# Optimization experiments

Measured on AMD Instinct MI355X. Metric: run time of the kernel, lower is better.

## Reference

```python
import jax, jax.numpy as jnp
import numpy as np

E = 1024
H = 16
D = E // H  # head dim = 64


def _moe(x, Wexp, bexp, Wg, bg):
    # x: (m, s, e); Wexp: (3, e, o); bexp: (3, o); Wg: (e, 3); bg: (3,)
    gate = jax.nn.softmax(jnp.einsum('mse,en->msn', x, Wg) + bg, axis=-1)  # (m,s,3)
    expert_out = jnp.einsum('mse,neo->msno', x, Wexp) + bexp               # (m,s,3,o)
    return jnp.einsum('msn,msno->mso', gate, expert_out)


def setup_inputs() -> dict:
    key = jax.random.key(0)
    ks = jax.random.split(key, 10)
    m, s = 4, 2048
    sc = 1.0 / np.sqrt(E)
    inp = {'x': jax.random.normal(ks[0], (m, s, E), jnp.float32)}
    for i, p in enumerate(['q', 'k', 'v']):
        inp['W' + p] = jax.random.normal(ks[1 + 3 * i], (3, E, E), jnp.float32) * sc
        inp['b' + p] = jnp.zeros((3, E), jnp.float32)
        inp['Wg' + p] = jax.random.normal(ks[2 + 3 * i], (E, 3), jnp.float32) * sc
        inp['bg' + p] = jnp.zeros((3,), jnp.float32)
    return inp


def reference(x, Wq, bq, Wgq, bgq, Wk, bk, Wgk, bgk, Wv, bv, Wgv, bgv):
    m, s, e = x.shape
    xq = _moe(x, Wq, bq, Wgq, bgq).reshape(m, s, H, D).transpose(0, 2, 1, 3)  # (m,H,s,D)
    xk = _moe(x, Wk, bk, Wgk, bgk).reshape(m, s, H, D).transpose(0, 2, 1, 3)
    xv = _moe(x, Wv, bv, Wgv, bgv).reshape(m, s, H, D).transpose(0, 2, 1, 3)
    scores = jnp.einsum('mhqd,mhkd->mhqk', xq, xk) / jnp.float32(np.sqrt(D))
    attn = jax.nn.softmax(scores, axis=-1)
    out = jnp.einsum('mhqk,mhkd->mhqd', attn, xv)
    return out.transpose(0, 2, 1, 3).reshape(m, s, e)
```

## Files before the change

kernel.cpp:

```cpp
#include <hip/hip_runtime.h>
#include <math.h>

#define T_TOK 8192
#define E_DIM 1024
#define S_LEN 2048

typedef _Float16 f16x4 __attribute__((ext_vector_type(4)));
typedef _Float16 f16x8 __attribute__((ext_vector_type(8)));
typedef float f32x16 __attribute__((ext_vector_type(16)));

__device__ __forceinline__ void async16(const void* g, void* l) {
  __builtin_amdgcn_global_load_lds(
      (const __attribute__((address_space(1))) void*)g,
      (__attribute__((address_space(3))) void*)l, 16, 0, 0);
}

__global__ __launch_bounds__(64) void gates_kernel(
    const float* __restrict__ x,
    const float* __restrict__ Wgq, const float* __restrict__ bgq,
    const float* __restrict__ Wgk, const float* __restrict__ bgk,
    const float* __restrict__ Wgv, const float* __restrict__ bgv,
    float* __restrict__ gates) {
  const int t = blockIdx.x;
  const int lane = threadIdx.x;
  const float* xr = x + (size_t)t * E_DIM;
  float acc[9];
#pragma unroll
  for (int i = 0; i < 9; ++i) acc[i] = 0.f;
  for (int e = lane; e < E_DIM; e += 64) {
    const float xv = xr[e];
    acc[0] = fmaf(xv, Wgq[e * 3 + 0], acc[0]);
    acc[1] = fmaf(xv, Wgq[e * 3 + 1], acc[1]);
    acc[2] = fmaf(xv, Wgq[e * 3 + 2], acc[2]);
    acc[3] = fmaf(xv, Wgk[e * 3 + 0], acc[3]);
    acc[4] = fmaf(xv, Wgk[e * 3 + 1], acc[4]);
    acc[5] = fmaf(xv, Wgk[e * 3 + 2], acc[5]);
    acc[6] = fmaf(xv, Wgv[e * 3 + 0], acc[6]);
    acc[7] = fmaf(xv, Wgv[e * 3 + 1], acc[7]);
    acc[8] = fmaf(xv, Wgv[e * 3 + 2], acc[8]);
  }
#pragma unroll
  for (int off = 32; off > 0; off >>= 1) {
#pragma unroll
    for (int i = 0; i < 9; ++i) acc[i] += __shfl_down(acc[i], off, 64);
  }
  if (lane == 0) {
    const float* bg[3] = {bgq, bgk, bgv};
#pragma unroll
    for (int p = 0; p < 3; ++p) {
      float z0 = acc[p * 3 + 0] + bg[p][0];
      float z1 = acc[p * 3 + 1] + bg[p][1];
      float z2 = acc[p * 3 + 2] + bg[p][2];
      float mx = fmaxf(z0, fmaxf(z1, z2));
      float e0 = expf(z0 - mx), e1 = expf(z1 - mx), e2 = expf(z2 - mx);
      float inv = 1.f / (e0 + e1 + e2);
      float* gp = gates + ((size_t)p * T_TOK + t) * 3;
      gp[0] = e0 * inv;
      gp[1] = e1 * inv;
      gp[2] = e2 * inv;
    }
  }
}

__global__ __launch_bounds__(256) void split_x_kernel(
    const float* __restrict__ x, _Float16* __restrict__ xh, _Float16* __restrict__ xl) {
  const size_t i = ((size_t)blockIdx.x * 256 + threadIdx.x) * 4;
  const float4 v = *(const float4*)(x + i);
  f16x4 h, lo;
  h[0] = (_Float16)v.x; lo[0] = (_Float16)(v.x - (float)h[0]);
  h[1] = (_Float16)v.y; lo[1] = (_Float16)(v.y - (float)h[1]);
  h[2] = (_Float16)v.z; lo[2] = (_Float16)(v.z - (float)h[2]);
  h[3] = (_Float16)v.w; lo[3] = (_Float16)(v.w - (float)h[3]);
  *(f16x4*)(xh + i) = h;
  *(f16x4*)(xl + i) = lo;
}

__global__ __launch_bounds__(256) void split_w_kernel(
    const float* __restrict__ Wq, const float* __restrict__ Wk, const float* __restrict__ Wv,
    _Float16* __restrict__ wh, _Float16* __restrict__ wl) {
  const int mat = blockIdx.y;
  const float* W = ((mat < 3) ? Wq : (mat < 6) ? Wk : Wv) + (size_t)(mat % 3) * 1048576;
  const int kt = (blockIdx.x >> 4) * 64, ct = (blockIdx.x & 15) * 64;
  __shared__ _Float16 hs[64][72];
  __shared__ _Float16 ls[64][72];
  const int tid = threadIdx.x;
#pragma unroll
  for (int i = 0; i < 4; ++i) {
    const int r = (tid >> 4) + i * 16;
    const int c4 = (tid & 15) * 4;
    const float4 v = *(const float4*)(W + (size_t)(kt + r) * 1024 + ct + c4);
    _Float16 h;
    h = (_Float16)v.x; hs[c4 + 0][r] = h; ls[c4 + 0][r] = (_Float16)(v.x - (float)h);
    h = (_Float16)v.y; hs[c4 + 1][r] = h; ls[c4 + 1][r] = (_Float16)(v.y - (float)h);
    h = (_Float16)v.z; hs[c4 + 2][r] = h; ls[c4 + 2][r] = (_Float16)(v.z - (float)h);
    h = (_Float16)v.w; hs[c4 + 3][r] = h; ls[c4 + 3][r] = (_Float16)(v.w - (float)h);
  }
  __syncthreads();
#pragma unroll
  for (int i = 0; i < 2; ++i) {
    const int u = tid + i * 256;
    const int c = u >> 3, seg = u & 7;
    const size_t o = (size_t)mat * 1048576 + (size_t)(ct + c) * 1024 + kt + seg * 8;
    *(f16x8*)(wh + o) = *(const f16x8*)(&hs[c][seg * 8]);
    *(f16x8*)(wl + o) = *(const f16x8*)(&ls[c][seg * 8]);
  }
}

__global__ __launch_bounds__(256, 2) void moe_mfma_kernel(
    const _Float16* __restrict__ xh, const _Float16* __restrict__ xl,
    const _Float16* __restrict__ wh, const _Float16* __restrict__ wl,
    const float* __restrict__ bq_, const float* __restrict__ bk_, const float* __restrict__ bv_,
    const float* __restrict__ gates,
    float* __restrict__ oq_, float* __restrict__ ok_, float* __restrict__ ov_) {
  const int p = blockIdx.z;
  const float* bias = (p == 0) ? bq_ : (p == 1) ? bk_ : bv_;
  float* out = (p == 0) ? oq_ : (p == 1) ? ok_ : ov_;

  __shared__ _Float16 Ah[128][32], Al[128][32], Bh[128][32], Bl[128][32];
  __shared__ float gsh[128][3];
  __shared__ float bsh[3][128];

  const int tid = threadIdx.x;
  const int l = tid & 63, w = tid >> 6;
  const int wm = w & 1, wn = w >> 1;
  const int row0 = blockIdx.x * 128, col0 = blockIdx.y * 128;

  for (int i = tid; i < 384; i += 256)
    gsh[i / 3][i % 3] = gates[((size_t)p * T_TOK + row0 + i / 3) * 3 + (i % 3)];
  for (int i = tid; i < 384; i += 256)
    bsh[i >> 7][i & 127] = bias[(i >> 7) * 1024 + col0 + (i & 127)];

  const int m = l & 31, half = l >> 5;
  const int S = (m >> 1) & 3;
  const int rr = l >> 2;
  const int gc = (l & 3) ^ ((l >> 3) & 3);
  const size_t aoff = (size_t)(row0 + w * 32 + rr) * 1024 + gc * 8;

  f32x16 fin[2][2];
#pragma unroll
  for (int i = 0; i < 2; ++i)
#pragma unroll
    for (int j = 0; j < 2; ++j)
#pragma unroll
      for (int r = 0; r < 16; ++r) fin[i][j][r] = 0.f;

  for (int e = 0; e < 3; ++e) {
    f32x16 acc[2][2];
#pragma unroll
    for (int i = 0; i < 2; ++i)
#pragma unroll
      for (int j = 0; j < 2; ++j)
#pragma unroll
        for (int r = 0; r < 16; ++r) acc[i][j][r] = 0.f;

    const size_t wbase = ((size_t)(p * 3 + e) * 1024 + col0 + w * 32 + rr) * 1024 + gc * 8;

    for (int ks = 0; ks < 32; ++ks) {
      const int k0 = ks * 32;
      __syncthreads();
      async16(xh + aoff + k0,             &Ah[w * 32][0]);
      async16(xh + aoff + k0 + 16 * 1024, &Ah[w * 32 + 16][0]);
      async16(xl + aoff + k0,             &Al[w * 32][0]);
      async16(xl + aoff + k0 + 16 * 1024, &Al[w * 32 + 16][0]);
      async16(wh + wbase + k0,             &Bh[w * 32][0]);
      async16(wh + wbase + k0 + 16 * 1024, &Bh[w * 32 + 16][0]);
      async16(wl + wbase + k0,             &Bl[w * 32][0]);
      async16(wl + wbase + k0 + 16 * 1024, &Bl[w * 32 + 16][0]);
      __syncthreads();

#pragma unroll
      for (int ss = 0; ss < 2; ++ss) {
        const int ch = ((ss << 1) | half) ^ S;
        f16x8 a_h[2], a_l[2], b_h[2], b_l[2];
#pragma unroll
        for (int i = 0; i < 2; ++i) {
          const int rA = wm * 64 + i * 32 + m;
          a_h[i] = *(const f16x8*)(&Ah[rA][ch * 8]);
          a_l[i] = *(const f16x8*)(&Al[rA][ch * 8]);
          const int rB = wn * 64 + i * 32 + m;
          b_h[i] = *(const f16x8*)(&Bh[rB][ch * 8]);
          b_l[i] = *(const f16x8*)(&Bl[rB][ch * 8]);
        }
#pragma unroll
        for (int i = 0; i < 2; ++i)
#pragma unroll
          for (int j = 0; j < 2; ++j) {
            acc[i][j] = __builtin_amdgcn_mfma_f32_32x32x16_f16(a_h[i], b_h[j], acc[i][j], 0, 0, 0);
            acc[i][j] = __builtin_amdgcn_mfma_f32_32x32x16_f16(a_h[i], b_l[j], acc[i][j], 0, 0, 0);
            acc[i][j] = __builtin_amdgcn_mfma_f32_32x32x16_f16(a_l[i], b_h[j], acc[i][j], 0, 0, 0);
          }
      }
    }
#pragma unroll
    for (int i = 0; i < 2; ++i)
#pragma unroll
      for (int r = 0; r < 16; ++r) {
        const int row_l = wm * 64 + i * 32 + (r & 3) + ((r >> 2) << 3) + (half << 2);
        const float g = gsh[row_l][e];
#pragma unroll
        for (int j = 0; j < 2; ++j) fin[i][j][r] += g * acc[i][j][r];
      }
  }

#pragma unroll
  for (int j = 0; j < 2; ++j) {
    const int col_l = wn * 64 + j * 32 + m;
    const float b0 = bsh[0][col_l], b1 = bsh[1][col_l], b2 = bsh[2][col_l];
#pragma unroll
    for (int i = 0; i < 2; ++i)
#pragma unroll
      for (int r = 0; r < 16; ++r) {
        const int row_l = wm * 64 + i * 32 + (r & 3) + ((r >> 2) << 3) + (half << 2);
        const float g0 = gsh[row_l][0], g1 = gsh[row_l][1], g2 = gsh[row_l][2];
        out[(size_t)(row0 + row_l) * 1024 + col0 + col_l] =
            fin[i][j][r] + g0 * b0 + g1 * b1 + g2 * b2;
      }
  }
}

__global__ __launch_bounds__(256) void repack_qk_kernel(
    const float* __restrict__ src, _Float16* __restrict__ h, _Float16* __restrict__ lo,
    float scale) {
  const size_t i = ((size_t)blockIdx.x * 256 + threadIdx.x) * 4;
  float4 v = *(const float4*)(src + i);
  v.x *= scale; v.y *= scale; v.z *= scale; v.w *= scale;
  const int t = (int)(i >> 10);
  const int e = (int)(i & 1023);
  const int d = e & 63, c = d >> 3, j = d & 7;
  const size_t dst = (i & ~(size_t)63) + (size_t)(((c ^ (t & 7)) << 3) | j);
  f16x4 hh, ll;
  hh[0] = (_Float16)v.x; ll[0] = (_Float16)(v.x - (float)hh[0]);
  hh[1] = (_Float16)v.y; ll[1] = (_Float16)(v.y - (float)hh[1]);
  hh[2] = (_Float16)v.z; ll[2] = (_Float16)(v.z - (float)hh[2]);
  hh[3] = (_Float16)v.w; ll[3] = (_Float16)(v.w - (float)hh[3]);
  *(f16x4*)(h + dst) = hh;
  *(f16x4*)(lo + dst) = ll;
}

__global__ __launch_bounds__(256) void repack_vT_kernel(
    const float* __restrict__ xv, _Float16* __restrict__ vth, _Float16* __restrict__ vtl) {
  const int mh = blockIdx.y;
  const int s0 = blockIdx.x * 64;
  __shared__ _Float16 hs[64][72];
  __shared__ _Float16 ls[64][72];
  const int tid = threadIdx.x;
#pragma unroll
  for (int i = 0; i < 4; ++i) {
    const int idx = tid + i * 256;
    const int sr = idx >> 4;
    const int c4 = (idx & 15) * 4;
    const float4 v = *(const float4*)(
        xv + ((size_t)(mh >> 4) * S_LEN + s0 + sr) * 1024 + (mh & 15) * 64 + c4);
    _Float16 h;
    h = (_Float16)v.x; hs[c4 + 0][sr] = h; ls[c4 + 0][sr] = (_Float16)(v.x - (float)h);
    h = (_Float16)v.y; hs[c4 + 1][sr] = h; ls[c4 + 1][sr] = (_Float16)(v.y - (float)h);
    h = (_Float16)v.z; hs[c4 + 2][sr] = h; ls[c4 + 2][sr] = (_Float16)(v.z - (float)h);
    h = (_Float16)v.w; hs[c4 + 3][sr] = h; ls[c4 + 3][sr] = (_Float16)(v.w - (float)h);
  }
  __syncthreads();
#pragma unroll
  for (int i = 0; i < 2; ++i) {
    const int u = tid + i * 256;
    const int d = u >> 3, kc = u & 7;
    const int phys = kc ^ (d & 7);
    const size_t o = ((size_t)mh * 64 + d) * (size_t)S_LEN + s0 + phys * 8;
    *(f16x8*)(vth + o) = *(const f16x8*)(&hs[d][kc * 8]);
    *(f16x8*)(vtl + o) = *(const f16x8*)(&ls[d][kc * 8]);
  }
}

__global__ __launch_bounds__(256, 3) void attn_mfma_kernel(
    const _Float16* __restrict__ qh, const _Float16* __restrict__ ql,
    const _Float16* __restrict__ kh, const _Float16* __restrict__ kl,
    const _Float16* __restrict__ vth, const _Float16* __restrict__ vtl,
    float* __restrict__ out) {
  __shared__ __align__(16) char KSraw[16640];
  __shared__ __align__(16) char QPraw[16384];
  __shared__ __align__(16) char VTraw[16384];
  __shared__ float alphas[64];
  __shared__ float lstate[64];

  _Float16* Kh = (_Float16*)KSraw;
  _Float16* Kl = Kh + 4096;
  float* Sb = (float*)KSraw;
  _Float16* Qh = (_Float16*)QPraw;
  _Float16* Ql = Qh + 4096;
  _Float16* VTh = (_Float16*)VTraw;
  _Float16* VTl = VTh + 4096;

  const int tid = threadIdx.x;
  const int l = tid & 63, w = tid >> 6;
  const int wm = w & 1, wn = w >> 1;
  const int m = l & 31, half = l >> 5;
  const int key = m & 7;
  const int qt0 = blockIdx.x * 64;
  const int mh = blockIdx.y;
  const int mi = mh >> 4, h = mh & 15;
  const size_t tok0 = (size_t)mi * S_LEN;

  const int r8 = l >> 3, c8 = l & 7;

  {
    const size_t g0 = (tok0 + qt0 + w * 16 + r8) * 1024 + h * 64 + c8 * 8;
    async16(qh + g0,            Qh + (w * 16) * 64);
    async16(qh + g0 + 8 * 1024, Qh + (w * 16 + 8) * 64);
    async16(ql + g0,            Ql + (w * 16) * 64);
    async16(ql + g0 + 8 * 1024, Ql + (w * 16 + 8) * 64);
  }
  __syncthreads();

  f16x8 qa_h[4], qa_l[4];
#pragma unroll
  for (int ks = 0; ks < 4; ++ks) {
    const int phys = (ks * 2 + half) ^ key;
    const int ro = (wm * 32 + m) * 64 + phys * 8;
    qa_h[ks] = *(const f16x8*)(Qh + ro);
    qa_l[ks] = *(const f16x8*)(Ql + ro);
  }

  const int sq = tid >> 2, part = tid & 3;
  const int k0 = part * 16;
  float mreg = -3.0e38f, lreg = 0.f;

  f32x16 o_acc;
#pragma unroll
  for (int r = 0; r < 16; ++r) o_acc[r] = 0.f;

  for (int jt = 0; jt < 32; ++jt) {
    const int kt0 = jt * 64;
    __syncthreads();

    {
      const size_t g0 = (tok0 + kt0 + w * 16 + r8) * 1024 + h * 64 + c8 * 8;
      async16(kh + g0,            Kh + (w * 16) * 64);
      async16(kh + g0 + 8 * 1024, Kh + (w * 16 + 8) * 64);
      async16(kl + g0,            Kl + (w * 16) * 64);
      async16(kl + g0 + 8 * 1024, Kl + (w * 16 + 8) * 64);
      const size_t v0 = ((size_t)mh * 64 + w * 16 + r8) * (size_t)S_LEN + kt0 + c8 * 8;
      async16(vth + v0,            VTh + (w * 16) * 64);
      async16(vth + v0 + 8 * 2048, VTh + (w * 16 + 8) * 64);
      async16(vtl + v0,            VTl + (w * 16) * 64);
      async16(vtl + v0 + 8 * 2048, VTl + (w * 16 + 8) * 64);
    }
    __syncthreads();

    f32x16 s_acc;
#pragma unroll
    for (int r = 0; r < 16; ++r) s_acc[r] = 0.f;
#pragma unroll
    for (int ks = 0; ks < 4; ++ks) {
      const int phys = (ks * 2 + half) ^ key;
      const int bo = (wn * 32 + m) * 64 + phys * 8;
      const f16x8 kb_h = *(const f16x8*)(Kh + bo);
      const f16x8 kb_l = *(const f16x8*)(Kl + bo);
      s_acc = __builtin_amdgcn_mfma_f32_32x32x16_f16(qa_h[ks], kb_h, s_acc, 0, 0, 0);
      s_acc = __builtin_amdgcn_mfma_f32_32x32x16_f16(qa_h[ks], kb_l, s_acc, 0, 0, 0);
      s_acc = __builtin_amdgcn_mfma_f32_32x32x16_f16(qa_l[ks], kb_h, s_acc, 0, 0, 0);
    }
    __syncthreads();

#pragma unroll
    for (int r = 0; r < 16; ++r) {
      const int row = wm * 32 + (r & 3) + ((r >> 2) << 3) + (half << 2);
      Sb[row * 65 + wn * 32 + m] = s_acc[r];
    }
    __syncthreads();

    {
      float pv[16];
      float mc = -3.0e38f;
#pragma unroll
      for (int k2 = 0; k2 < 16; ++k2) {
        pv[k2] = Sb[sq * 65 + k0 + k2];
        mc = fmaxf(mc, pv[k2]);
      }
      mc = fmaxf(mc, __shfl_xor(mc, 1, 64));
      mc = fmaxf(mc, __shfl_xor(mc, 2, 64));
      const float mn = fmaxf(mreg, mc);
      float rs = 0.f;
#pragma unroll
      for (int k2 = 0; k2 < 16; ++k2) {
        const float pe = __expf(pv[k2] - mn);
        pv[k2] = pe;
        rs += pe;
      }
      rs += __shfl_xor(rs, 1, 64);
      rs += __shfl_xor(rs, 2, 64);
      const float al = __expf(mreg - mn);
      lreg = lreg * al + rs;
      mreg = mn;
      if (part == 0) alphas[sq] = al;
      const int skey = sq & 7;
      f16x8 p_h, p_l;
#pragma unroll
      for (int z = 0; z < 8; ++z) {
        p_h[z] = (_Float16)pv[z];
        p_l[z] = (_Float16)(pv[z] - (float)p_h[z]);
      }
      int phys = (2 * part) ^ skey;
      *(f16x8*)(Qh + sq * 64 + phys * 8) = p_h;
      *(f16x8*)(Ql + sq * 64 + phys * 8) = p_l;
#pragma unroll
      for (int z = 0; z < 8; ++z) {
        p_h[z] = (_Float16)pv[8 + z];
        p_l[z] = (_Float16)(pv[8 + z] - (float)p_h[z]);
      }
      phys = (2 * part + 1) ^ skey;
      *(f16x8*)(Qh + sq * 64 + phys * 8) = p_h;
      *(f16x8*)(Ql + sq * 64 + phys * 8) = p_l;
    }
    __syncthreads();

#pragma unroll
    for (int r = 0; r < 16; ++r) {
      const int row = wm * 32 + (r & 3) + ((r >> 2) << 3) + (half << 2);
      o_acc[r] *= alphas[row];
    }
#pragma unroll
    for (int ks = 0; ks < 4; ++ks) {
      const int phys = (ks * 2 + half) ^ key;
      const int po = (wm * 32 + m) * 64 + phys * 8;
      const f16x8 pa_h = *(const f16x8*)(Qh + po);
      const f16x8 pa_l = *(const f16x8*)(Ql + po);
      const int vo = (wn * 32 + m) * 64 + phys * 8;
      const f16x8 vb_h = *(const f16x8*)(VTh + vo);
      const f16x8 vb_l = *(const f16x8*)(VTl + vo);
      o_acc = __builtin_amdgcn_mfma_f32_32x32x16_f16(pa_h, vb_h, o_acc, 0, 0, 0);
      o_acc = __builtin_amdgcn_mfma_f32_32x32x16_f16(pa_h, vb_l, o_acc, 0, 0, 0);
      o_acc = __builtin_amdgcn_mfma_f32_32x32x16_f16(pa_l, vb_h, o_acc, 0, 0, 0);
    }
  }

  if (part == 0) lstate[sq] = lreg;
  __syncthreads();
#pragma unroll
  for (int r = 0; r < 16; ++r) {
    const int row = wm * 32 + (r & 3) + ((r >> 2) << 3) + (half << 2);
    const float linv = 1.f / lstate[row];
    out[(tok0 + qt0 + row) * 1024 + h * 64 + wn * 32 + m] = o_acc[r] * linv;
  }
}

__global__ __launch_bounds__(256) void moe_gemm_kernel(
    const float* __restrict__ x,
    const float* __restrict__ Wq_, const float* __restrict__ bq_,
    const float* __restrict__ Wk_, const float* __restrict__ bk_,
    const float* __restrict__ Wv_, const float* __restrict__ bv_,
    const float* __restrict__ gates,
    float* __restrict__ oq_, float* __restrict__ ok_, float* __restrict__ ov_) {
  const int p = blockIdx.z;
  const float* W = (p == 0) ? Wq_ : (p == 1) ? Wk_ : Wv_;
  const float* bias = (p == 0) ? bq_ : (p == 1) ? bk_ : bv_;
  float* out = (p == 0) ? oq_ : (p == 1) ? ok_ : ov_;
  const float* gbase = gates + (size_t)p * T_TOK * 3;

  __shared__ float AsT[8][128];
  __shared__ float Bs[8][128];
  __shared__ float gsh[128][3];

  const int tid = threadIdx.x;
  const int tx = tid & 15;
  const int ty = tid >> 4;
  const int row0 = blockIdx.x * 128;
  const int col0 = blockIdx.y * 128;

  for (int i = tid; i < 384; i += 256)
    gsh[i / 3][i % 3] = gbase[(size_t)(row0 + i / 3) * 3 + (i % 3)];

  float acc[8][8];
#pragma unroll
  for (int i = 0; i < 8; ++i)
#pragma unroll
    for (int j = 0; j < 8; ++j) acc[i][j] = 0.f;

  __syncthreads();

  const int ar = tid >> 1;
  const int ac = (tid & 1) << 2;
  const int br = tid >> 5;
  const int bc = (tid & 31) << 2;
  const float* xrow = x + (size_t)(row0 + ar) * E_DIM + ac;

  for (int kk = 0; kk < 3072; kk += 8) {
    const int n = kk >> 10;
    const int k = kk & 1023;
    const float g = gsh[ar][n];
    const float4 av = *(const float4*)(xrow + k);
    AsT[ac + 0][ar] = av.x * g;
    AsT[ac + 1][ar] = av.y * g;
    AsT[ac + 2][ar] = av.z * g;
    AsT[ac + 3][ar] = av.w * g;
    *(float4*)(&Bs[br][bc]) =
        *(const float4*)(W + (size_t)n * 1048576 + (size_t)(k + br) * 1024 + col0 + bc);
    __syncthreads();
#pragma unroll
    for (int kq = 0; kq < 8; ++kq) {
      const float4 a0 = *(const float4*)(&AsT[kq][ty * 4]);
      const float4 a1 = *(const float4*)(&AsT[kq][64 + ty * 4]);
      const float4 b0 = *(const float4*)(&Bs[kq][tx * 4]);
      const float4 b1 = *(const float4*)(&Bs[kq][64 + tx * 4]);
      const float a[8] = {a0.x, a0.y, a0.z, a0.w, a1.x, a1.y, a1.z, a1.w};
      const float b[8] = {b0.x, b0.y, b0.z, b0.w, b1.x, b1.y, b1.z, b1.w};
#pragma unroll
      for (int i = 0; i < 8; ++i)
#pragma unroll
        for (int j = 0; j < 8; ++j) acc[i][j] = fmaf(a[i], b[j], acc[i][j]);
    }
    __syncthreads();
  }

#pragma unroll
  for (int ih = 0; ih < 2; ++ih) {
#pragma unroll
    for (int i = 0; i < 4; ++i) {
      const int rl = ih * 64 + ty * 4 + i;
      const float g0 = gsh[rl][0], g1 = gsh[rl][1], g2 = gsh[rl][2];
      float* orow = out + (size_t)(row0 + rl) * E_DIM;
#pragma unroll
      for (int jh = 0; jh < 2; ++jh) {
        const int cl = jh * 64 + tx * 4;
        const int c = col0 + cl;
        float4 v;
        v.x = acc[ih * 4 + i][jh * 4 + 0] + g0 * bias[c + 0] + g1 * bias[1024 + c + 0] + g2 * bias[2048 + c + 0];
        v.y = acc[ih * 4 + i][jh * 4 + 1] + g0 * bias[c + 1] + g1 * bias[1024 + c + 1] + g2 * bias[2048 + c + 1];
        v.z = acc[ih * 4 + i][jh * 4 + 2] + g0 * bias[c + 2] + g1 * bias[1024 + c + 2] + g2 * bias[2048 + c + 2];
        v.w = acc[ih * 4 + i][jh * 4 + 3] + g0 * bias[c + 3] + g1 * bias[1024 + c + 3] + g2 * bias[2048 + c + 3];
        *(float4*)(orow + c) = v;
      }
    }
  }
}

__global__ __launch_bounds__(256) void attn_kernel(
    const float* __restrict__ xq, const float* __restrict__ xk,
    const float* __restrict__ xv, float* __restrict__ out) {
  __shared__ float QsT[64][64];
  __shared__ float KsT[64][64];
  __shared__ float Vs[64][64];
  __shared__ float Ss[64][65];
  __shared__ float mstate[64], lstate[64], alphas[64];

  const int tid = threadIdx.x;
  const int tx = tid & 15;
  const int ty = tid >> 4;
  const int qt0 = blockIdx.x * 64;
  const int mh = blockIdx.y;
  const int mi = mh >> 4, h = mh & 15;
  const size_t base = ((size_t)mi * S_LEN) * E_DIM + (size_t)h * 64;

  for (int it = tid; it < 1024; it += 256) {
    const int row = it >> 4, c4 = (it & 15) << 2;
    const float4 qv = *(const float4*)(xq + base + (size_t)(qt0 + row) * E_DIM + c4);
    QsT[c4 + 0][row] = qv.x;
    QsT[c4 + 1][row] = qv.y;
    QsT[c4 + 2][row] = qv.z;
    QsT[c4 + 3][row] = qv.w;
  }
  if (tid < 64) {
    mstate[tid] = -3.0e38f;
    lstate[tid] = 0.f;
  }
  float o[4][4];
#pragma unroll
  for (int i = 0; i < 4; ++i)
#pragma unroll
    for (int j = 0; j < 4; ++j) o[i][j] = 0.f;

  for (int jt = 0; jt < 32; ++jt) {
    __syncthreads();
    const int kt0 = jt * 64;
    for (int it = tid; it < 1024; it += 256) {
      const int row = it >> 4, c4 = (it & 15) << 2;
      const size_t ga = base + (size_t)(kt0 + row) * E_DIM + c4;
      const float4 kv = *(const float4*)(xk + ga);
      KsT[c4 + 0][row] = kv.x;
      KsT[c4 + 1][row] = kv.y;
      KsT[c4 + 2][row] = kv.z;
      KsT[c4 + 3][row] = kv.w;
      *(float4*)(&Vs[row][c4]) = *(const float4*)(xv + ga);
    }
    __syncthreads();

    float s[4][4];
#pragma unroll
    for (int i = 0; i < 4; ++i)
#pragma unroll
      for (int j = 0; j < 4; ++j) s[i][j] = 0.f;
#pragma unroll 8
    for (int d = 0; d < 64; ++d) {
      const float4 a4 = *(const float4*)(&QsT[d][ty * 4]);
      const float4 b4 = *(const float4*)(&KsT[d][tx * 4]);
      const float a[4] = {a4.x, a4.y, a4.z, a4.w};
      const float b[4] = {b4.x, b4.y, b4.z, b4.w};
#pragma unroll
      for (int i = 0; i < 4; ++i)
#pragma unroll
        for (int j = 0; j < 4; ++j) s[i][j] = fmaf(a[i], b[j], s[i][j]);
    }
#pragma unroll
    for (int i = 0; i < 4; ++i)
#pragma unroll
      for (int j = 0; j < 4; ++j) Ss[ty * 4 + i][tx * 4 + j] = s[i][j] * 0.125f;
    __syncthreads();

    {
      const int q = tid >> 2, part = tid & 3;
      const int k0 = part * 16;
      const float mprev = mstate[q];
      float mcur = -3.0e38f;
#pragma unroll
      for (int k2 = 0; k2 < 16; ++k2) mcur = fmaxf(mcur, Ss[q][k0 + k2]);
      mcur = fmaxf(mcur, __shfl_xor(mcur, 1, 64));
      mcur = fmaxf(mcur, __shfl_xor(mcur, 2, 64));
      const float mnew = fmaxf(mprev, mcur);
      float rs = 0.f;
#pragma unroll
      for (int k2 = 0; k2 < 16; ++k2) {
        const float pv = __expf(Ss[q][k0 + k2] - mnew);
        Ss[q][k0 + k2] = pv;
        rs += pv;
      }
      rs += __shfl_xor(rs, 1, 64);
      rs += __shfl_xor(rs, 2, 64);
      if (part == 0) {
        const float alpha = __expf(mprev - mnew);
        lstate[q] = lstate[q] * alpha + rs;
        mstate[q] = mnew;
        alphas[q] = alpha;
      }
    }
    __syncthreads();

    float al[4];
#pragma unroll
    for (int i = 0; i < 4; ++i) al[i] = alphas[ty * 4 + i];
#pragma unroll
    for (int i = 0; i < 4; ++i)
#pragma unroll
      for (int j = 0; j < 4; ++j) o[i][j] *= al[i];
#pragma unroll 8
    for (int k2 = 0; k2 < 64; ++k2) {
      float pr[4];
#pragma unroll
      for (int i = 0; i < 4; ++i) pr[i] = Ss[ty * 4 + i][k2];
      const float4 v4 = *(const float4*)(&Vs[k2][tx * 4]);
#pragma unroll
      for (int i = 0; i < 4; ++i) {
        o[i][0] = fmaf(pr[i], v4.x, o[i][0]);
        o[i][1] = fmaf(pr[i], v4.y, o[i][1]);
        o[i][2] = fmaf(pr[i], v4.z, o[i][2]);
        o[i][3] = fmaf(pr[i], v4.w, o[i][3]);
      }
    }
  }

#pragma unroll
  for (int i = 0; i < 4; ++i) {
    const float linv = 1.f / lstate[ty * 4 + i];
    float4 v;
    v.x = o[i][0] * linv;
    v.y = o[i][1] * linv;
    v.z = o[i][2] * linv;
    v.w = o[i][3] * linv;
    *(float4*)(out + base + (size_t)(qt0 + ty * 4 + i) * E_DIM + tx * 4) = v;
  }
}

extern "C" void kernel_launch(void* const* d_in, const int* in_sizes, int n_in,
                              void* d_out, int out_size, void* d_ws, size_t ws_size,
                              hipStream_t stream) {
  (void)in_sizes; (void)n_in; (void)out_size;
  const float* x   = (const float*)d_in[0];
  const float* Wq  = (const float*)d_in[1];
  const float* bq  = (const float*)d_in[2];
  const float* Wgq = (const float*)d_in[3];
  const float* bgq = (const float*)d_in[4];
  const float* Wk  = (const float*)d_in[5];
  const float* bk  = (const float*)d_in[6];
  const float* Wgk = (const float*)d_in[7];
  const float* bgk = (const float*)d_in[8];
  const float* Wv  = (const float*)d_in[9];
  const float* bv  = (const float*)d_in[10];
  const float* Wgv = (const float*)d_in[11];
  const float* bgv = (const float*)d_in[12];
  float* out = (float*)d_out;

  const size_t off_xsh = 294912;
  const size_t off_xsl = off_xsh + 16777216;
  const size_t off_wth = off_xsl + 16777216;
  const size_t off_wtl = off_wth + 18874368;
  const size_t off_xq  = off_wtl + 18874368;
  const size_t need_mfma = off_xq + 3ull * 33554432;
  const size_t need_f32  = 294912 + 3ull * 33554432;

  float* gates = (float*)d_ws;

  if (ws_size >= need_mfma) {
    _Float16* xsh = (_Float16*)((char*)d_ws + off_xsh);
    _Float16* xsl = (_Float16*)((char*)d_ws + off_xsl);
    _Float16* wth = (_Float16*)((char*)d_ws + off_wth);
    _Float16* wtl = (_Float16*)((char*)d_ws + off_wtl);
    float* xq = (float*)((char*)d_ws + off_xq);
    float* xk = xq + (size_t)T_TOK * E_DIM;
    float* xv = xk + (size_t)T_TOK * E_DIM;
    _Float16* qh  = xsh;
    _Float16* ql  = xsl;
    _Float16* khb = wth;
    _Float16* klb = wtl;
    _Float16* vth = (_Float16*)((char*)d_ws + off_xq);
    _Float16* vtl = vth + 8388608;

    split_x_kernel<<<dim3(8192), dim3(256), 0, stream>>>(x, xsh, xsl);
    split_w_kernel<<<dim3(256, 9), dim3(256), 0, stream>>>(Wq, Wk, Wv, wth, wtl);
    gates_kernel<<<dim3(T_TOK), dim3(64), 0, stream>>>(x, Wgq, bgq, Wgk, bgk, Wgv, bgv, gates);
    moe_mfma_kernel<<<dim3(T_TOK / 128, E_DIM / 128, 3), dim3(256), 0, stream>>>(
        xsh, xsl, wth, wtl, bq, bk, bv, gates, xq, xk, xv);
    repack_qk_kernel<<<dim3(8192), dim3(256), 0, stream>>>(xq, qh, ql, 0.125f);
    repack_qk_kernel<<<dim3(8192), dim3(256), 0, stream>>>(xk, khb, klb, 1.0f);
    repack_vT_kernel<<<dim3(32, 64), dim3(256), 0, stream>>>(xv, vth, vtl);
    attn_mfma_kernel<<<dim3(32, 64), dim3(256), 0, stream>>>(qh, ql, khb, klb, vth, vtl, out);
  } else if (ws_size >= need_f32) {
    float* xq = (float*)((char*)d_ws + 294912);
    float* xk = xq + (size_t)T_TOK * E_DIM;
    float* xv = xk + (size_t)T_TOK * E_DIM;
    gates_kernel<<<dim3(T_TOK), dim3(64), 0, stream>>>(x, Wgq, bgq, Wgk, bgk, Wgv, bgv, gates);
    moe_gemm_kernel<<<dim3(T_TOK / 128, E_DIM / 128, 3), dim3(256), 0, stream>>>(
        x, Wq, bq, Wk, bk, Wv, bv, gates, xq, xk, xv);
    attn_kernel<<<dim3(S_LEN / 64, 64), dim3(256), 0, stream>>>(xq, xk, xv, out);
  }
}
```

Baseline: 968.7 us.

## Double-buffer LDS tiles and prefetch across a flattened expert-K loop

The shared-memory tiles for the hi/lo fp16 A and B operands become ping-pong buffers, and the three-expert by 32-K-step nest becomes a single 96-step loop. Each iteration issues async global-to-LDS loads for the next step before running the MFMAs on the current buffer, so memory latency can overlap compute and one barrier per step is dropped. Gate scaling into the final accumulator happens every 32 steps inside the loop. The cost is double the LDS footprint (about 64KB per block), which may limit occupancy, plus extra branch logic in the loop body.

```diff
diff --git a/kernel.cpp b/kernel.cpp
--- a/kernel.cpp
+++ b/kernel.cpp
@@ -116,7 +116,8 @@
   const float* bias = (p == 0) ? bq_ : (p == 1) ? bk_ : bv_;
   float* out = (p == 0) ? oq_ : (p == 1) ? ok_ : ov_;
 
-  __shared__ _Float16 Ah[128][32], Al[128][32], Bh[128][32], Bl[128][32];
+  __shared__ _Float16 Ah[2][128][32], Al[2][128][32];
+  __shared__ _Float16 Bh[2][128][32], Bl[2][128][32];
   __shared__ float gsh[128][3];
   __shared__ float bsh[3][128];
 
@@ -135,71 +136,76 @@
   const int rr = l >> 2;
   const int gc = (l & 3) ^ ((l >> 3) & 3);
   const size_t aoff = (size_t)(row0 + w * 32 + rr) * 1024 + gc * 8;
-
-  f32x16 fin[2][2];
+  const size_t wcol = ((size_t)col0 + w * 32 + rr) * 1024 + gc * 8;
+
+  auto stage = [&](int seq, int buf) {
+    const int e = seq >> 5;
+    const int k0 = (seq & 31) << 5;
+    const size_t wb = (size_t)(p * 3 + e) * 1048576 + wcol;
+    async16(xh + aoff + k0,             &Ah[buf][w * 32][0]);
+    async16(xh + aoff + k0 + 16 * 1024, &Ah[buf][w * 32 + 16][0]);
+    async16(xl + aoff + k0,             &Al[buf][w * 32][0]);
+    async16(xl + aoff + k0 + 16 * 1024, &Al[buf][w * 32 + 16][0]);
+    async16(wh + wb + k0,               &Bh[buf][w * 32][0]);
+    async16(wh + wb + k0 + 16 * 1024,   &Bh[buf][w * 32 + 16][0]);
+    async16(wl + wb + k0,               &Bl[buf][w * 32][0]);
+    async16(wl + wb + k0 + 16 * 1024,   &Bl[buf][w * 32 + 16][0]);
+  };
+
+  f32x16 fin[2][2], acc[2][2];
 #pragma unroll
   for (int i = 0; i < 2; ++i)
 #pragma unroll
     for (int j = 0; j < 2; ++j)
 #pragma unroll
-      for (int r = 0; r < 16; ++r) fin[i][j][r] = 0.f;
-
-  for (int e = 0; e < 3; ++e) {
-    f32x16 acc[2][2];
-#pragma unroll
-    for (int i = 0; i < 2; ++i)
-#pragma unroll
-      for (int j = 0; j < 2; ++j)
-#pragma unroll
-        for (int r = 0; r < 16; ++r) acc[i][j][r] = 0.f;
-
-    const size_t wbase = ((size_t)(p * 3 + e) * 1024 + col0 + w * 32 + rr) * 1024 + gc * 8;
-
-    for (int ks = 0; ks < 32; ++ks) {
-      const int k0 = ks * 32;
-      __syncthreads();
-      async16(xh + aoff + k0,             &Ah[w * 32][0]);
-      async16(xh + aoff + k0 + 16 * 1024, &Ah[w * 32 + 16][0]);
-      async16(xl + aoff + k0,             &Al[w * 32][0]);
-      async16(xl + aoff + k0 + 16 * 1024, &Al[w * 32 + 16][0]);
-      async16(wh + wbase + k0,             &Bh[w * 32][0]);
-      async16(wh + wbase + k0 + 16 * 1024, &Bh[w * 32 + 16][0]);
-      async16(wl + wbase + k0,             &Bl[w * 32][0]);
-      async16(wl + wbase + k0 + 16 * 1024, &Bl[w * 32 + 16][0]);
-      __syncthreads();
-
-#pragma unroll
-      for (int ss = 0; ss < 2; ++ss) {
-        const int ch = ((ss << 1) | half) ^ S;
-        f16x8 a_h[2], a_l[2], b_h[2], b_l[2];
-#pragma unroll
-        for (int i = 0; i < 2; ++i) {
-          const int rA = wm * 64 + i * 32 + m;
-          a_h[i] = *(const f16x8*)(&Ah[rA][ch * 8]);
-          a_l[i] = *(const f16x8*)(&Al[rA][ch * 8]);
-          const int rB = wn * 64 + i * 32 + m;
-          b_h[i] = *(const f16x8*)(&Bh[rB][ch * 8]);
-          b_l[i] = *(const f16x8*)(&Bl[rB][ch * 8]);
+      for (int r = 0; r < 16; ++r) { fin[i][j][r] = 0.f; acc[i][j][r] = 0.f; }
+
+  stage(0, 0);
+
+#pragma unroll 2
+  for (int seq = 0; seq < 96; ++seq) {
+    const int buf = seq & 1;
+    __syncthreads();
+    if (seq < 95) stage(seq + 1, buf ^ 1);
+
+#pragma unroll
+    for (int ss = 0; ss < 2; ++ss) {
+      const int ch = ((ss << 1) | half) ^ S;
+      f16x8 a_h[2], a_l[2], b_h[2], b_l[2];
+#pragma unroll
+      for (int i = 0; i < 2; ++i) {
+        const int rA = wm * 64 + i * 32 + m;
+        a_h[i] = *(const f16x8*)(&Ah[buf][rA][ch * 8]);
+        a_l[i] = *(const f16x8*)(&Al[buf][rA][ch * 8]);
+        const int rB = wn * 64 + i * 32 + m;
+        b_h[i] = *(const f16x8*)(&Bh[buf][rB][ch * 8]);
+        b_l[i] = *(const f16x8*)(&Bl[buf][rB][ch * 8]);
+      }
+#pragma unroll
+      for (int i = 0; i < 2; ++i)
+#pragma unroll
+        for (int j = 0; j < 2; ++j) {
+          acc[i][j] = __builtin_amdgcn_mfma_f32_32x32x16_f16(a_h[i], b_h[j], acc[i][j], 0, 0, 0);
+          acc[i][j] = __builtin_amdgcn_mfma_f32_32x32x16_f16(a_h[i], b_l[j], acc[i][j], 0, 0, 0);
+          acc[i][j] = __builtin_amdgcn_mfma_f32_32x32x16_f16(a_l[i], b_h[j], acc[i][j], 0, 0, 0);
         }
-#pragma unroll
-        for (int i = 0; i < 2; ++i)
+    }
+
+    if ((seq & 31) == 31) {
+      const int e = seq >> 5;
+#pragma unroll
+      for (int i = 0; i < 2; ++i)
+#pragma unroll
+        for (int r = 0; r < 16; ++r) {
+          const int row_l = wm * 64 + i * 32 + (r & 3) + ((r >> 2) << 3) + (half << 2);
+          const float g = gsh[row_l][e];
 #pragma unroll
           for (int j = 0; j < 2; ++j) {
-            acc[i][j] = __builtin_amdgcn_mfma_f32_32x32x16_f16(a_h[i], b_h[j], acc[i][j], 0, 0, 0);
-            acc[i][j] = __builtin_amdgcn_mfma_f32_32x32x16_f16(a_h[i], b_l[j], acc[i][j], 0, 0, 0);
-            acc[i][j] = __builtin_amdgcn_mfma_f32_32x32x16_f16(a_l[i], b_h[j], acc[i][j], 0, 0, 0);
+            fin[i][j][r] += g * acc[i][j][r];
+            acc[i][j][r] = 0.f;
           }
-      }
-    }
-#pragma unroll
-    for (int i = 0; i < 2; ++i)
-#pragma unroll
-      for (int r = 0; r < 16; ++r) {
-        const int row_l = wm * 64 + i * 32 + (r & 3) + ((r >> 2) << 3) + (half << 2);
-        const float g = gsh[row_l][e];
-#pragma unroll
-        for (int j = 0; j < 2; ++j) fin[i][j][r] += g * acc[i][j][r];
-      }
+        }
+    }
   }
 
 #pragma unroll
```

Result: no change. 951.9 us (-1.7%).
